# Kernel tuning notes

Measured on AMD Instinct MI355X. Metric: run time of the kernel, lower is better.

Reference implementation:

```python
import jax, jax.numpy as jnp
import numpy as np

B, S, D, H = 4, 4096, 1024, 64

def setup_inputs() -> dict:
    key = jax.random.key(0)
    k1, k2, k3, k4 = jax.random.split(key, 4)
    inp = {
        'input': jax.random.normal(k1, (B, S, D), dtype=jnp.float32),
        'Wq': jax.random.normal(k2, (D, H), dtype=jnp.float32) * (D ** -0.5),
        'Wk': jax.random.normal(k3, (D, H), dtype=jnp.float32) * (D ** -0.5),
        'Wv': jax.random.normal(k4, (D, H), dtype=jnp.float32) * (D ** -0.5),
    }
    return inp

def reference(input, Wq, Wk, Wv):
    # Projections: [B,S,D] @ [D,H] -> [B,S,H]
    q = input @ Wq
    k = input @ Wk
    v = input @ Wv
    head_size = Wq.shape[-1]
    # Scaled scores: [B,S,S]
    scores = jnp.einsum('bqh,bkh->bqk', q, k) * (head_size ** -0.5)
    seq_len = input.shape[1]
    causal = jnp.tril(jnp.ones((seq_len, seq_len), dtype=bool))
    masked = jnp.where(causal, scores, -jnp.inf)
    weights = jax.nn.softmax(masked, axis=-1)
    # dropout p=0.0 -> identity
    return jnp.einsum('bqk,bkh->bqh', weights, v)
```

## Files before the change

### kernel.cpp

```cpp
#include <hip/hip_runtime.h>

#define NS 8

typedef __attribute__((ext_vector_type(8))) short sh8;
typedef __attribute__((ext_vector_type(4))) short sh4;
typedef __attribute__((ext_vector_type(4))) float f4;

#define QSCALE 0.18033688011112042f

static __device__ __forceinline__ unsigned short f2bf(float f) {
  unsigned u = __builtin_bit_cast(unsigned, f);
  u += 0x7fffu + ((u >> 16) & 1u);
  return (unsigned short)(u >> 16);
}
static __device__ __forceinline__ float bf2f(unsigned short s) {
  unsigned u = ((unsigned)s) << 16;
  return __builtin_bit_cast(float, u);
}

__global__ __launch_bounds__(256) void wt_kernel(const float* __restrict__ Wq,
                                                 const float* __restrict__ Wk,
                                                 const float* __restrict__ Wv,
                                                 unsigned short* __restrict__ Wt2) {
  int blk = blockIdx.x;
  int band = blk >> 3;
  int widx = band >> 2;
  const float* W = widx == 0 ? Wq : (widx == 1 ? Wk : Wv);
  int ncol = (band & 3) * 16;
  int t = threadIdx.x;
  int kt = (blk & 7) * 4 + (t >> 6);
  int lane = t & 63, q = lane >> 4, l15 = lane & 15;
  const float* src = W + (size_t)(kt * 32 + q * 8) * 64 + ncol + l15;
  sh8 o;
#pragma unroll
  for (int j = 0; j < 8; ++j) o[j] = (short)f2bf(src[(size_t)j * 64]);
  *(sh8*)&Wt2[((size_t)(band * 32 + kt) * 64 + lane) * 8] = o;
}

__global__ __launch_bounds__(256, 4) void proj_kernel(const float* __restrict__ in,
                                                      const unsigned short* __restrict__ Wt2,
                                                      unsigned short* __restrict__ Qg,
                                                      unsigned short* __restrict__ Kg,
                                                      unsigned short* __restrict__ Vtg) {
  int t = threadIdx.x;
  int w = t >> 6, lane = t & 63, q = lane >> 4, l15 = lane & 15;
  int m0 = blockIdx.x * 16;

  const float* arow = in + (size_t)(m0 + l15) * 1024 + q * 8;
  const unsigned short* bbase = Wt2 + (size_t)(w * 3) * 16384 + lane * 8;

  f4 acc[3];
  f4 z = {0.f, 0.f, 0.f, 0.f};
#pragma unroll
  for (int nt = 0; nt < 3; ++nt) acc[nt] = z;

#pragma unroll 4
  for (int kt = 0; kt < 32; ++kt) {
    f4 lo = *(const f4*)(arow + kt * 32);
    f4 hi = *(const f4*)(arow + kt * 32 + 4);
    sh8 a;
#pragma unroll
    for (int j = 0; j < 4; ++j) {
      a[j] = (short)f2bf(lo[j]);
      a[4 + j] = (short)f2bf(hi[j]);
    }
#pragma unroll
    for (int nt = 0; nt < 3; ++nt) {
      sh8 bf = *(const sh8*)(bbase + nt * 16384 + kt * 512);
      acc[nt] = __builtin_amdgcn_mfma_f32_16x16x32_bf16(a, bf, acc[nt], 0, 0, 0);
    }
  }

  int bb = m0 >> 12, s0 = m0 & 4095;
#pragma unroll
  for (int nt = 0; nt < 3; ++nt) {
    int band = w * 3 + nt;
    if (band < 4) {
#pragma unroll
      for (int r = 0; r < 4; ++r)
        Qg[(size_t)(m0 + q * 4 + r) * 64 + band * 16 + l15] = f2bf(acc[nt][r] * QSCALE);
    } else if (band < 8) {
#pragma unroll
      for (int r = 0; r < 4; ++r)
        Kg[(size_t)(m0 + q * 4 + r) * 64 + (band - 4) * 16 + l15] = f2bf(acc[nt][r]);
    } else {
      int h = (band - 8) * 16 + l15;
      sh4 pv;
#pragma unroll
      for (int r = 0; r < 4; ++r) pv[r] = (short)f2bf(acc[nt][r]);
      *(sh4*)&Vtg[(((size_t)(bb * 64 + h)) << 12) + s0 + q * 4] = pv;
    }
  }
}

__global__ __launch_bounds__(256, 4) void attn_split(const unsigned short* __restrict__ Qg,
                                                     const unsigned short* __restrict__ Kg,
                                                     const unsigned short* __restrict__ Vtg,
                                                     unsigned short* __restrict__ Opart,
                                                     float* __restrict__ Lpart) {
  __shared__ unsigned short Ks[64 * 72];
  __shared__ unsigned short Vs[64 * 72];
  __shared__ unsigned short Pw[4 * 16 * 72];
  int t = threadIdx.x;
  int b = blockIdx.y;
  int qt = 63 - (int)(blockIdx.x >> 3);
  int sp = blockIdx.x & 7;
  int wave = t >> 6, lane = t & 63, quad = lane >> 4, l15 = lane & 15;
  unsigned short* Pws = Pw + wave * 16 * 72;

  int qrow0 = qt * 64 + wave * 16;
  size_t pbase = ((size_t)sp * 4 + b) * 4096;

  int nkt = qt + 1;
  int chunk = (nkt + NS - 1) / NS;
  int t0 = sp * chunk, t1 = min(nkt, t0 + chunk);
  if (t0 >= t1) {
#pragma unroll
    for (int r = 0; r < 4; ++r) {
      size_t row = pbase + qrow0 + quad * 4 + r;
#pragma unroll
      for (int ht = 0; ht < 4; ++ht) Opart[row * 64 + ht * 16 + l15] = 0;
      if (l15 == 0) Lpart[row] = 0.f;
    }
    return;
  }

  sh8 qa[2];
#pragma unroll
  for (int ks = 0; ks < 2; ++ks)
    qa[ks] = *(const sh8*)&Qg[(size_t)((b << 12) + qrow0 + l15) * 64 + ks * 32 + quad * 8];

  sh8 ones;
#pragma unroll
  for (int j = 0; j < 8; ++j) ones[j] = (short)0x3F80;

  f4 o[5];
  f4 z = {0.f, 0.f, 0.f, 0.f};
#pragma unroll
  for (int ht = 0; ht < 5; ++ht) o[ht] = z;

  int r0 = t >> 3, o0 = (t & 7) * 8;
  int r1 = (t + 256) >> 3, o1 = ((t + 256) & 7) * 8;
  const unsigned short* kg0 = Kg + (size_t)((b << 12) + r0) * 64 + o0;
  const unsigned short* kg1 = Kg + (size_t)((b << 12) + r1) * 64 + o1;
  const unsigned short* vg0 = Vtg + (((size_t)(b * 64 + r0)) << 12) + o0;
  const unsigned short* vg1 = Vtg + (((size_t)(b * 64 + r1)) << 12) + o1;

  sh8 kr0, kr1, vr0, vr1;
  {
    size_t ko = (size_t)t0 * 64 * 64;
    kr0 = *(const sh8*)(kg0 + ko); kr1 = *(const sh8*)(kg1 + ko);
    vr0 = *(const sh8*)(vg0 + t0 * 64); vr1 = *(const sh8*)(vg1 + t0 * 64);
  }

  for (int kt = t0; kt < t1; ++kt) {
    __syncthreads();
    *(sh8*)&Ks[r0 * 72 + o0] = kr0;
    *(sh8*)&Ks[r1 * 72 + o1] = kr1;
    *(sh8*)&Vs[r0 * 72 + o0] = vr0;
    *(sh8*)&Vs[r1 * 72 + o1] = vr1;
    if (kt + 1 < t1) {
      size_t ko = (size_t)(kt + 1) * 64 * 64;
      kr0 = *(const sh8*)(kg0 + ko); kr1 = *(const sh8*)(kg1 + ko);
      vr0 = *(const sh8*)(vg0 + (kt + 1) * 64); vr1 = *(const sh8*)(vg1 + (kt + 1) * 64);
    }
    __syncthreads();

    f4 st[4];
#pragma unroll
    for (int nt = 0; nt < 4; ++nt) st[nt] = z;
#pragma unroll
    for (int ks = 0; ks < 2; ++ks) {
#pragma unroll
      for (int nt = 0; nt < 4; ++nt) {
        sh8 kb = *(const sh8*)&Ks[(nt * 16 + l15) * 72 + ks * 32 + quad * 8];
        st[nt] = __builtin_amdgcn_mfma_f32_16x16x32_bf16(kb, qa[ks], st[nt], 0, 0, 0);
      }
    }

    if (kt == nkt - 1) {
      int qrow = qrow0 + l15;
#pragma unroll
      for (int nt = 0; nt < 4; ++nt) {
        int key0 = kt * 64 + nt * 16 + quad * 4;
#pragma unroll
        for (int r = 0; r < 4; ++r)
          if (key0 + r > qrow) st[nt][r] = -__builtin_inff();
      }
    }

#pragma unroll
    for (int nt = 0; nt < 4; ++nt) {
      sh4 pk;
#pragma unroll
      for (int r = 0; r < 4; ++r) pk[r] = (short)f2bf(exp2f(st[nt][r]));
      *(sh4*)&Pws[l15 * 72 + nt * 16 + quad * 4] = pk;
    }
    asm volatile("s_waitcnt lgkmcnt(0)" ::: "memory");

#pragma unroll
    for (int ks = 0; ks < 2; ++ks) {
      sh8 pa = *(const sh8*)&Pws[l15 * 72 + ks * 32 + quad * 8];
#pragma unroll
      for (int ht = 0; ht < 4; ++ht) {
        sh8 vb = *(const sh8*)&Vs[(ht * 16 + l15) * 72 + ks * 32 + quad * 8];
        o[ht] = __builtin_amdgcn_mfma_f32_16x16x32_bf16(pa, vb, o[ht], 0, 0, 0);
      }
      o[4] = __builtin_amdgcn_mfma_f32_16x16x32_bf16(pa, ones, o[4], 0, 0, 0);
    }
  }

#pragma unroll
  for (int r = 0; r < 4; ++r) {
    size_t row = pbase + qrow0 + quad * 4 + r;
#pragma unroll
    for (int ht = 0; ht < 4; ++ht)
      Opart[row * 64 + ht * 16 + l15] = f2bf(o[ht][r]);
    if (l15 == 0) Lpart[row] = o[4][r];
  }
}

__global__ __launch_bounds__(256) void attn_combine(const unsigned short* __restrict__ Opart,
                                                    const float* __restrict__ Lpart,
                                                    float* __restrict__ out) {
  int t = threadIdx.x;
  int rg = blockIdx.x * 4 + (t >> 6);
  int lane = t & 63;
  float acc = 0.f, L = 0.f;
#pragma unroll
  for (int s = 0; s < NS; ++s) {
    L += Lpart[(size_t)s * 16384 + rg];
    acc += bf2f(Opart[((size_t)s * 16384 + rg) * 64 + lane]);
  }
  out[(size_t)rg * 64 + lane] = acc / L;
}

extern "C" void kernel_launch(void* const* d_in, const int* in_sizes, int n_in,
                              void* d_out, int out_size, void* d_ws, size_t ws_size,
                              hipStream_t stream) {
  const float* in = (const float*)d_in[0];
  const float* Wq = (const float*)d_in[1];
  const float* Wk = (const float*)d_in[2];
  const float* Wv = (const float*)d_in[3];
  float* out = (float*)d_out;

  char* ws = (char*)d_ws;
  unsigned short* Wt2   = (unsigned short*)ws;
  unsigned short* Qg    = (unsigned short*)(ws + 393216);
  unsigned short* Kg    = (unsigned short*)(ws + 2490368);
  unsigned short* Vtg   = (unsigned short*)(ws + 4587520);
  unsigned short* Opart = (unsigned short*)(ws + 6684672);
  float*          Lpart = (float*)(ws + 23461888);

  hipLaunchKernelGGL(wt_kernel, dim3(96), dim3(256), 0, stream, Wq, Wk, Wv, Wt2);
  hipLaunchKernelGGL(proj_kernel, dim3(1024), dim3(256), 0, stream, in, Wt2, Qg, Kg, Vtg);
  hipLaunchKernelGGL(attn_split, dim3(64 * NS, 4), dim3(256), 0, stream,
                     Qg, Kg, Vtg, Opart, Lpart);
  hipLaunchKernelGGL(attn_combine, dim3(4096), dim3(256), 0, stream,
                     Opart, Lpart, out);
}
```

Measured before the change: 164.9 us.

## Double-buffer projection operands via global_load_lds and transpose V through LDS

The projection kernel now stages each K-slice of the fp32 input rows and the bf16 weight fragments into LDS with asynchronous global_load_lds. It uses two buffers so the next slice's loads overlap the current MFMAs, with one block barrier per iteration. The V output is first written to an LDS scratch tile and then read back transposed, so each thread stores a contiguous 4-element chunk of Vt. This adds barriers and LDS traffic, and relies on the compiler emitting correct vmcnt waits before each barrier.

```diff
diff --git a/kernel.cpp b/kernel.cpp
--- a/kernel.cpp
+++ b/kernel.cpp
@@ -7,6 +7,10 @@
 typedef __attribute__((ext_vector_type(4))) float f4;
 
 #define QSCALE 0.18033688011112042f
+
+typedef const __attribute__((address_space(1))) unsigned int* gas_t;
+typedef __attribute__((address_space(3))) unsigned int* las_t;
+#define GLD16(g, l) __builtin_amdgcn_global_load_lds((gas_t)(g), (las_t)(l), 16, 0, 0)
 
 static __device__ __forceinline__ unsigned short f2bf(float f) {
   unsigned u = __builtin_bit_cast(unsigned, f);
@@ -42,54 +46,77 @@
                                                       unsigned short* __restrict__ Qg,
                                                       unsigned short* __restrict__ Kg,
                                                       unsigned short* __restrict__ Vtg) {
+  __shared__ __align__(16) char lds[28672];
   int t = threadIdx.x;
   int w = t >> 6, lane = t & 63, q = lane >> 4, l15 = lane & 15;
   int m0 = blockIdx.x * 16;
 
-  const float* arow = in + (size_t)(m0 + l15) * 1024 + q * 8;
-  const unsigned short* bbase = Wt2 + (size_t)(w * 3) * 16384 + lane * 8;
+  const float* ga = in + (size_t)(m0 + l15) * 1024 + q * 8 + (w & 1) * 4;
+  const unsigned short* gb = Wt2 + (size_t)(w * 3) * 16384 + lane * 8;
 
   f4 acc[3];
   f4 z = {0.f, 0.f, 0.f, 0.f};
 #pragma unroll
   for (int nt = 0; nt < 3; ++nt) acc[nt] = z;
 
-#pragma unroll 4
+#define STAGE(kt, buf)                                                        \
+  {                                                                           \
+    int k0 = (kt) * 32;                                                       \
+    char* base = lds + (buf) * 14336;                                         \
+    if (w < 2) GLD16(ga + k0, base + w * 1024);                               \
+    GLD16(gb + (kt) * 512, base + 2048 + (w * 3 + 0) * 1024);                 \
+    GLD16(gb + 16384 + (kt) * 512, base + 2048 + (w * 3 + 1) * 1024);         \
+    GLD16(gb + 32768 + (kt) * 512, base + 2048 + (w * 3 + 2) * 1024);         \
+  }
+
+  STAGE(0, 0);
   for (int kt = 0; kt < 32; ++kt) {
-    f4 lo = *(const f4*)(arow + kt * 32);
-    f4 hi = *(const f4*)(arow + kt * 32 + 4);
+    int cur = kt & 1;
+    __syncthreads();
+    if (kt + 1 < 32) STAGE(kt + 1, cur ^ 1);
+
+    const f4* Af = (const f4*)(lds + cur * 14336);
+    f4 lo = Af[lane], hi = Af[64 + lane];
     sh8 a;
 #pragma unroll
     for (int j = 0; j < 4; ++j) {
       a[j] = (short)f2bf(lo[j]);
       a[4 + j] = (short)f2bf(hi[j]);
     }
+    const sh8* Bf = (const sh8*)(lds + cur * 14336 + 2048);
 #pragma unroll
     for (int nt = 0; nt < 3; ++nt) {
-      sh8 bf = *(const sh8*)(bbase + nt * 16384 + kt * 512);
+      sh8 bf = Bf[(w * 3 + nt) * 64 + lane];
       acc[nt] = __builtin_amdgcn_mfma_f32_16x16x32_bf16(a, bf, acc[nt], 0, 0, 0);
     }
   }
-
-  int bb = m0 >> 12, s0 = m0 & 4095;
+#undef STAGE
+
+  float* vred = (float*)lds;
 #pragma unroll
   for (int nt = 0; nt < 3; ++nt) {
     int band = w * 3 + nt;
-    if (band < 4) {
-#pragma unroll
-      for (int r = 0; r < 4; ++r)
-        Qg[(size_t)(m0 + q * 4 + r) * 64 + band * 16 + l15] = f2bf(acc[nt][r] * QSCALE);
-    } else if (band < 8) {
-#pragma unroll
-      for (int r = 0; r < 4; ++r)
-        Kg[(size_t)(m0 + q * 4 + r) * 64 + (band - 4) * 16 + l15] = f2bf(acc[nt][r]);
-    } else {
-      int h = (band - 8) * 16 + l15;
-      sh4 pv;
-#pragma unroll
-      for (int r = 0; r < 4; ++r) pv[r] = (short)f2bf(acc[nt][r]);
-      *(sh4*)&Vtg[(((size_t)(bb * 64 + h)) << 12) + s0 + q * 4] = pv;
-    }
+#pragma unroll
+    for (int r = 0; r < 4; ++r) {
+      int row = q * 4 + r;
+      float v = acc[nt][r];
+      if (band < 4) {
+        Qg[(size_t)(m0 + row) * 64 + band * 16 + l15] = f2bf(v * QSCALE);
+      } else if (band < 8) {
+        Kg[(size_t)(m0 + row) * 64 + (band - 4) * 16 + l15] = f2bf(v);
+      } else {
+        vred[row * 69 + (band - 8) * 16 + l15] = v;
+      }
+    }
+  }
+  __syncthreads();
+  {
+    int h = t >> 2, sl = (t & 3) * 4;
+    int bb = m0 >> 12, s0 = m0 & 4095;
+    sh4 vv;
+#pragma unroll
+    for (int j = 0; j < 4; ++j) vv[j] = (short)f2bf(vred[(sl + j) * 69 + h]);
+    *(sh4*)&Vtg[(((size_t)(bb * 64 + h)) << 12) + s0 + sl] = vv;
   }
 }
 
```

Result: faster. 153.7 us (-6.8%).
